# Kernel optimization log

Hardware: AMD Instinct MI355X
Metric: run time of the kernel (lower is better)

Reference implementation:

```python
import jax, jax.numpy as jnp
import numpy as np

# ---- static skeleton topology (20 edges, humanoid: spine + 2 arms + 2 legs) ----
EDGES = [(0,1),(1,2),(2,3),(3,4),(3,5),(5,6),(6,7),(7,8),(3,9),(9,10),(10,11),(11,12),
         (0,13),(13,14),(14,15),(15,16),(0,17),(17,18),(18,19),(19,20)]
SKELETON_DIST = 2
IN_PER_J, OUT_PER_J = 64, 128
KSIZE, PAD, STRIDE = 15, 7, 2
BATCH, T = 8, 4096


def _calc_edge_mat(edges):
    n = len(edges)
    INF = 100000
    m = np.full((n, n), INF, dtype=np.int64)
    np.fill_diagonal(m, 0)
    for i, a in enumerate(edges):
        for j, b in enumerate(edges):
            if a[0] in b or a[1] in b:
                m[i, j] = min(m[i, j], 1)
    for k in range(n):  # Floyd-Warshall on tiny static graph
        m = np.minimum(m, m[:, k:k+1] + m[k:k+1, :])
    return m


def _find_neighbor(edges, d):
    m = _calc_edge_mat(edges)
    n = len(edges)
    neigh = [[j for j in range(n) if m[i, j] <= d] for i in range(n)]
    global_part = list(neigh[0])
    for i in global_part:
        neigh[i].append(n)  # virtual global edge index n
    neigh.append(global_part)
    return neigh


def _build_mask(neigh, in_pj, out_pj, k):
    J = len(neigh)
    mask = np.zeros((J * out_pj, J * in_pj, k), dtype=np.float32)
    for i, nb in enumerate(neigh):
        for j in nb:
            mask[i*out_pj:(i+1)*out_pj, j*in_pj:(j+1)*in_pj, :] = 1.0
    return mask


def _build_pool_weight(edges, cpe):
    degree = [0] * 100
    for e in edges:
        degree[e[0]] += 1
        degree[e[1]] += 1
    seq_list = []
    def find_seq(j, seq):
        if degree[j] > 2 and j != 0:
            seq_list.append(seq); seq = []
        if degree[j] == 1:
            seq_list.append(seq); return
        for idx, e in enumerate(edges):
            if e[0] == j:
                find_seq(e[1], seq + [idx])
    find_seq(0, [])
    pooling = []
    for seq in seq_list:
        seq = list(seq)
        if len(seq) % 2 == 1:
            pooling.append([seq[0]]); seq = seq[1:]
        for i in range(0, len(seq), 2):
            pooling.append([seq[i], seq[i+1]])
    edge_num = len(edges) + 1
    pooling.append([edge_num - 1])
    W = np.zeros((len(pooling) * cpe, edge_num * cpe), dtype=np.float32)
    for i, pair in enumerate(pooling):
        for j in pair:
            for c in range(cpe):
                W[i*cpe + c, j*cpe + c] = 1.0 / len(pair)
    return W


def setup_inputs() -> dict:
    key = jax.random.key(0)
    k1, k2, k3 = jax.random.split(key, 3)
    J = len(EDGES) + 1  # 21 (edges + virtual global)
    in_c, out_c = J * IN_PER_J, J * OUT_PER_J  # 1344, 2688
    neigh = _find_neighbor(EDGES, SKELETON_DIST)
    mask = jnp.asarray(_build_mask(neigh, IN_PER_J, OUT_PER_J, KSIZE))
    pool_w = jnp.asarray(_build_pool_weight(EDGES, out_c // J))
    x = jax.random.normal(k1, (BATCH, in_c, T), dtype=jnp.float32)
    weight = jax.random.normal(k2, (out_c, in_c, KSIZE), dtype=jnp.float32) * 0.02
    bias = jax.random.normal(k3, (out_c,), dtype=jnp.float32) * 0.01
    return {"x": x, "weight": weight, "bias": bias, "mask": mask, "pool_w": pool_w}


def reference(x, weight, bias, mask, pool_w):
    # SkeletonConv: per-joint neighbor mask applied to dense conv1d weights
    w = weight * mask  # [out_c, in_c, K]
    xp = jnp.pad(x, ((0, 0), (0, 0), (PAD, PAD)), mode='reflect')
    y = jax.lax.conv_general_dilated(
        xp, w, window_strides=(STRIDE,), padding='VALID',
        dimension_numbers=('NCH', 'OIH', 'NCH'))
    y = y + bias[None, :, None]  # [B, out_c, T//2]
    # SkeletonPool: mean over graph-defined edge groups via matmul
    p = jnp.einsum('pc,bct->bpt', pool_w, y)
    # LeakyReLU activation as in the layer stack
    return jax.nn.leaky_relu(p, negative_slope=0.2)
```

## Files before the change

kernel.cpp:

```cpp
#include <hip/hip_runtime.h>
#include <cstdint>
#include <cstddef>

typedef unsigned short u16;
typedef unsigned int   u32;

typedef __bf16 bf16x8 __attribute__((ext_vector_type(8)));
typedef float  f32x4  __attribute__((ext_vector_type(4)));

#define AS1C(p) ((const __attribute__((address_space(1))) void*)(p))
#define AS3(p)  ((__attribute__((address_space(3))) void*)(p))

__constant__ int d_slot_jb[85] = {
  0,1,2,12,13,16,17,20,
  0,1,2,3,4,5,8,9,12,16,20,
  1,2,3,4,5,8,9,
  1,2,3,4,5,6,7,8,9,
  4,5,6,7,
  1,2,3,4,5,8,9,10,11,
  8,9,10,11,
  0,1,12,13,14,15,16,17,20,
  12,13,14,15,
  0,1,12,13,16,17,18,19,20,
  16,17,18,19,
  0,1,2,12,13,16,17
};
__constant__ int   d_gs0[12]    = {0,8,19,26,35,39,48,52,61,65,74,78};
__constant__ int   d_gnb[12]    = {8,11,7,9,4,9,4,9,4,9,4,7};
__constant__ int   d_gj0[12]    = {0,1,3,4,6,8,10,12,14,16,18,20};
__constant__ int   d_gj1[12]    = {-1,2,-1,5,7,9,11,13,15,17,19,-1};
__constant__ float d_gscale[12] = {1.f,0.5f,1.f,0.5f,0.5f,0.5f,0.5f,0.5f,0.5f,0.5f,0.5f,1.f};
__constant__ int   d_sched[12]  = {1,3,5,7,9,0,2,11,4,6,8,10};

static __device__ __forceinline__ u16 f2bf(float f) {
  union { float f; u32 u; } v; v.f = f;
  u32 r = v.u + 0x7fffu + ((v.u >> 16) & 1u);
  return (u16)(r >> 16);
}

__global__ void prep_x(const float* __restrict__ x, u16* __restrict__ xp) {
  int gid = blockIdx.x * 256 + threadIdx.x;
  if (gid >= 8 * 1344 * 514) return;
  int pc  = gid % 514;
  int row = gid / 514;
  int p   = pc * 8;
  const float* xr = x + (size_t)row * 4096;
  u16 v[8];
#pragma unroll
  for (int e = 0; e < 8; ++e) {
    int j = p + e - 7;
    j = j < 0 ? -j : (j > 4095 ? 8190 - j : j);
    v[e] = f2bf(xr[j]);
  }
  *(uint4*)(xp + (size_t)row * 4112 + p) = *(const uint4*)v;
}

__global__ void prep_w(const float* __restrict__ wt, const float* __restrict__ msk,
                       u16* __restrict__ apk) {
  int gid = blockIdx.x * 256 + threadIdx.x;
  if (gid >= 85 * 8192) return;
  int u   = gid >> 13;
  int rem = gid & 8191;
  int m   = rem >> 6;
  int c   = rem & 63;
  int g = 11;
#pragma unroll
  for (int gg = 0; gg < 11; ++gg)
    if (u >= d_gs0[gg] && u < d_gs0[gg + 1]) g = gg;
  int jb = d_slot_jb[u];
  int j0 = d_gj0[g], j1 = d_gj1[g];
  float sc = d_gscale[g];
  float m0 = msk[((size_t)(j0 * 128) * 1344 + jb * 64) * 15];
  float m1 = (j1 >= 0) ? msk[((size_t)(j1 * 128) * 1344 + jb * 64) * 15] : 0.f;
  const float* w0 = wt + ((size_t)(j0 * 128 + m) * 1344 + jb * 64 + c) * 15;
  const float* w1 = (j1 >= 0) ? wt + ((size_t)(j1 * 128 + m) * 1344 + jb * 64 + c) * 15 : w0;
  u16 v[16];
#pragma unroll
  for (int k = 0; k < 15; ++k) {
    float a = m0 * w0[k] + m1 * w1[k];
    v[k] = f2bf(a * sc);
  }
  v[15] = 0;
  uint4* dst = (uint4*)(apk + (size_t)u * 131072 + m * 1024 + c * 16);
  dst[0] = ((const uint4*)v)[0];
  dst[1] = ((const uint4*)v)[1];
}

__global__ void prep_b(const float* __restrict__ bias, float* __restrict__ bg) {
  int pc = blockIdx.x * 256 + threadIdx.x;
  if (pc >= 1536) return;
  int g = pc >> 7, m = pc & 127;
  float v = bias[d_gj0[g] * 128 + m];
  if (d_gj1[g] >= 0) v += bias[d_gj1[g] * 128 + m];
  bg[pc] = v * d_gscale[g];
}

__global__ __launch_bounds__(256, 3)
void conv_main(const u16* __restrict__ xpbf, const u16* __restrict__ apk,
               const float* __restrict__ biasg, float* __restrict__ out) {
  __shared__ __align__(16) u16 xs[64 * 280];
  __shared__ __align__(16) u16 as[128 * 64];

  const int tid = threadIdx.x;
  const int l   = tid & 63, w = tid >> 6;
  const int q   = l >> 4, lm = l & 15;
  const int wm  = w & 1, wn = w >> 1;

  const int gidx = blockIdx.x >> 7;
  const int g    = d_sched[gidx];
  const int r    = blockIdx.x & 127;
  const int b    = r >> 4;
  const int tile = r & 15;
  const int t0   = tile << 7;
  const int p0   = t0 << 1;

  const int nb = d_gnb[g];
  const int s0 = d_gs0[g];

  f32x4 acc[4][4];
#pragma unroll
  for (int i = 0; i < 4; ++i)
#pragma unroll
    for (int j = 0; j < 4; ++j)
      acc[i][j] = (f32x4){0.f, 0.f, 0.f, 0.f};

  const int as_mb = tid >> 3;
  const int as_sp = tid & 7;

  for (int s = 0; s < nb; ++s) {
    const int u  = s0 + s;
    const int jb = d_slot_jb[u];
    __syncthreads();
    {
      const u16* srow = xpbf + (size_t)(b * 1344 + jb * 64) * 4112 + p0;
      for (int i = tid; i < 64 * 34; i += 256) {
        int c  = i / 34;
        int sg = i - c * 34;
        uint4 v = *(const uint4*)(srow + (size_t)c * 4112 + sg * 8);
        *(uint4*)((char*)xs + c * 560 + sg * 16) = v;
      }
    }
    const u16* ablk = apk + (size_t)u * 131072;
    for (int kc = 0; kc < 16; ++kc) {
      __syncthreads();
#pragma unroll
      for (int ii = 0; ii < 4; ++ii) {
        int m    = ii * 32 + as_mb;
        int sloc = as_sp ^ (m & 7);
        const u16* gp = ablk + m * 1024 + kc * 64 + sloc * 8;
        __builtin_amdgcn_global_load_lds(AS1C(gp),
                                         AS3((char*)as + ii * 4096 + w * 1024),
                                         16, 0, 0);
      }
      __syncthreads();
#pragma unroll
      for (int ks = 0; ks < 2; ++ks) {
        bf16x8 af[4];
#pragma unroll
        for (int mt = 0; mt < 4; ++mt) {
          int m  = wm * 64 + mt * 16 + lm;
          int sp = (ks * 4 + q) ^ (m & 7);
          af[mt] = *(const bf16x8*)((const char*)as + m * 128 + sp * 16);
        }
        const int crow = kc * 4 + ks * 2 + (q >> 1);
        const char* xrow = (const char*)xs + crow * 560 + 16 * (q & 1);
#pragma unroll
        for (int nt = 0; nt < 4; ++nt) {
          int n = wn * 64 + nt * 16 + lm;
          const char* bp = xrow + 4 * n;
          union { u32 u[4]; bf16x8 v; } bb;
#pragma unroll
          for (int ww = 0; ww < 4; ++ww)
            bb.u[ww] = *(const u32*)(bp + 4 * ww);
#pragma unroll
          for (int mt = 0; mt < 4; ++mt)
            acc[mt][nt] = __builtin_amdgcn_mfma_f32_16x16x32_bf16(
                af[mt], bb.v, acc[mt][nt], 0, 0, 0);
        }
      }
    }
  }

  const float* bgp = biasg + g * 128 + wm * 64;
  float* outb = out + ((size_t)b * 1536 + g * 128 + wm * 64) * 2048 + t0 + wn * 64;
#pragma unroll
  for (int mt = 0; mt < 4; ++mt) {
    const f32x4 bv = *(const f32x4*)(bgp + mt * 16 + q * 4);
#pragma unroll
    for (int reg = 0; reg < 4; ++reg) {
      const float bias = bv[reg];
      const int m = mt * 16 + q * 4 + reg;
      float* orow = outb + (size_t)m * 2048 + lm;
#pragma unroll
      for (int nt = 0; nt < 4; ++nt) {
        float v = acc[mt][nt][reg] + bias;
        orow[nt * 16] = v < 0.f ? 0.2f * v : v;
      }
    }
  }
}

extern "C" void kernel_launch(void* const* d_in, const int* in_sizes, int n_in,
                              void* d_out, int out_size, void* d_ws, size_t ws_size,
                              hipStream_t stream) {
  (void)in_sizes; (void)n_in; (void)out_size; (void)ws_size;
  const float* x   = (const float*)d_in[0];
  const float* wt  = (const float*)d_in[1];
  const float* bs  = (const float*)d_in[2];
  const float* msk = (const float*)d_in[3];

  u16*   xpbf = (u16*)d_ws;
  u16*   apk  = (u16*)((char*)d_ws + 88424448);
  float* bg   = (float*)((char*)d_ws + 110706688);
  float* out  = (float*)d_out;

  prep_x<<<dim3(21588), dim3(256), 0, stream>>>(x, xpbf);
  prep_w<<<dim3(2720),  dim3(256), 0, stream>>>(wt, msk, apk);
  prep_b<<<dim3(6),     dim3(256), 0, stream>>>(bs, bg);
  conv_main<<<dim3(1536), dim3(256), 0, stream>>>(xpbf, apk, bg, out);
}
```

Baseline: 780.3 us.

## Coalesce prep_x and prep_w loads via LDS staging

prep_x now handles one row per block. It loads the row with float4 reads, packs it to bf16 in LDS, and writes the reflect-padded output using a shift-based fast path for interior chunks. prep_w now maps one wavefront to one output row (u,m), reads the 960 contiguous weights coalesced, and transposes them through LDS into the padded 16-tap layout. Both changes replace strided or scattered global reads with coalesced ones, at the cost of extra LDS traffic and a barrier per block.

```diff
diff --git a/kernel.cpp b/kernel.cpp
--- a/kernel.cpp
+++ b/kernel.cpp
@@ -37,53 +37,95 @@
   u32 r = v.u + 0x7fffu + ((v.u >> 16) & 1u);
   return (u16)(r >> 16);
 }
-
-__global__ void prep_x(const float* __restrict__ x, u16* __restrict__ xp) {
-  int gid = blockIdx.x * 256 + threadIdx.x;
-  if (gid >= 8 * 1344 * 514) return;
-  int pc  = gid % 514;
-  int row = gid / 514;
-  int p   = pc * 8;
-  const float* xr = x + (size_t)row * 4096;
-  u16 v[8];
-#pragma unroll
-  for (int e = 0; e < 8; ++e) {
-    int j = p + e - 7;
-    j = j < 0 ? -j : (j > 4095 ? 8190 - j : j);
-    v[e] = f2bf(xr[j]);
-  }
-  *(uint4*)(xp + (size_t)row * 4112 + p) = *(const uint4*)v;
-}
-
-__global__ void prep_w(const float* __restrict__ wt, const float* __restrict__ msk,
-                       u16* __restrict__ apk) {
-  int gid = blockIdx.x * 256 + threadIdx.x;
-  if (gid >= 85 * 8192) return;
-  int u   = gid >> 13;
-  int rem = gid & 8191;
-  int m   = rem >> 6;
-  int c   = rem & 63;
+static __device__ __forceinline__ u32 pk2(float lo, float hi) {
+  return (u32)f2bf(lo) | ((u32)f2bf(hi) << 16);
+}
+
+__global__ __launch_bounds__(256) void prep_x(const float* __restrict__ x,
+                                              u16* __restrict__ xp) {
+  __shared__ __align__(16) u32 lx[2048];
+  const int row = blockIdx.x;
+  const int t   = threadIdx.x;
+
+  {
+    const float4* xr4 = (const float4*)(x + (size_t)row * 4096) + t * 4;
+    float4 f0 = xr4[0], f1 = xr4[1], f2 = xr4[2], f3 = xr4[3];
+    u32 o[8];
+    o[0] = pk2(f0.x, f0.y); o[1] = pk2(f0.z, f0.w);
+    o[2] = pk2(f1.x, f1.y); o[3] = pk2(f1.z, f1.w);
+    o[4] = pk2(f2.x, f2.y); o[5] = pk2(f2.z, f2.w);
+    o[6] = pk2(f3.x, f3.y); o[7] = pk2(f3.z, f3.w);
+    ((uint4*)lx)[t * 2 + 0] = ((const uint4*)o)[0];
+    ((uint4*)lx)[t * 2 + 1] = ((const uint4*)o)[1];
+  }
+  __syncthreads();
+
+  u16* orow = xp + (size_t)row * 4112;
+  auto store_chunk = [&](int d) {
+    if (d >= 1 && d <= 511) {
+      uint4 A = ((const uint4*)lx)[d - 1];
+      u32  C = lx[4 * d];
+      uint4 o;
+      o.x = (A.x >> 16) | (A.y << 16);
+      o.y = (A.y >> 16) | (A.z << 16);
+      o.z = (A.z >> 16) | (A.w << 16);
+      o.w = (A.w >> 16) | (C << 16);
+      *(uint4*)(orow + d * 8) = o;
+    } else {
+      u32 o[4];
+#pragma unroll
+      for (int j = 0; j < 4; ++j) {
+        int p0 = d * 8 + 2 * j;
+        int s0 = p0 - 7; s0 = s0 < 0 ? -s0 : (s0 > 4095 ? 8190 - s0 : s0);
+        int s1 = p0 - 6; s1 = s1 < 0 ? -s1 : (s1 > 4095 ? 8190 - s1 : s1);
+        u32 w0 = lx[s0 >> 1], w1 = lx[s1 >> 1];
+        u32 lo = (s0 & 1) ? (w0 >> 16) : (w0 & 0xffffu);
+        u32 hi = (s1 & 1) ? (w1 >> 16) : (w1 & 0xffffu);
+        o[j] = lo | (hi << 16);
+      }
+      *(uint4*)(orow + d * 8) = ((const uint4*)o)[0];
+    }
+  };
+  store_chunk(t);
+  store_chunk(t + 256);
+  if (t < 2) store_chunk(512 + t);
+}
+
+__global__ __launch_bounds__(256) void prep_w(const float* __restrict__ wt,
+                                              const float* __restrict__ msk,
+                                              u16* __restrict__ apk) {
+  __shared__ float wls[4][1024];
+  const int t = threadIdx.x & 63, w = threadIdx.x >> 6;
+  const int wid = blockIdx.x * 4 + w;
+  const int u = wid >> 7, m = wid & 127;
   int g = 11;
 #pragma unroll
   for (int gg = 0; gg < 11; ++gg)
     if (u >= d_gs0[gg] && u < d_gs0[gg + 1]) g = gg;
-  int jb = d_slot_jb[u];
-  int j0 = d_gj0[g], j1 = d_gj1[g];
-  float sc = d_gscale[g];
-  float m0 = msk[((size_t)(j0 * 128) * 1344 + jb * 64) * 15];
-  float m1 = (j1 >= 0) ? msk[((size_t)(j1 * 128) * 1344 + jb * 64) * 15] : 0.f;
-  const float* w0 = wt + ((size_t)(j0 * 128 + m) * 1344 + jb * 64 + c) * 15;
-  const float* w1 = (j1 >= 0) ? wt + ((size_t)(j1 * 128 + m) * 1344 + jb * 64 + c) * 15 : w0;
-  u16 v[16];
+  const int jb = d_slot_jb[u];
+  const int j0 = d_gj0[g], j1 = d_gj1[g];
+  const float sc = d_gscale[g];
+  const float m0 = msk[((size_t)(j0 * 128) * 1344 + jb * 64) * 15] * sc;
+  const float m1 = (j1 >= 0) ? msk[((size_t)(j1 * 128) * 1344 + jb * 64) * 15] * sc : 0.f;
+  const float* w0 = wt + ((size_t)(j0 * 128 + m) * 1344 + jb * 64) * 15;
+  const float* w1 = (j1 >= 0) ? wt + ((size_t)(j1 * 128 + m) * 1344 + jb * 64) * 15 : w0;
+
+  float* L = wls[w];
+  L[t * 16 + 15] = 0.f;
 #pragma unroll
   for (int k = 0; k < 15; ++k) {
-    float a = m0 * w0[k] + m1 * w1[k];
-    v[k] = f2bf(a * sc);
-  }
-  v[15] = 0;
-  uint4* dst = (uint4*)(apk + (size_t)u * 131072 + m * 1024 + c * 16);
-  dst[0] = ((const uint4*)v)[0];
-  dst[1] = ((const uint4*)v)[1];
+    int i = k * 64 + t;
+    float v = m0 * w0[i] + m1 * w1[i];
+    int c = i / 15, tap = i - c * 15;
+    L[c * 16 + tap] = v;
+  }
+  __syncthreads();
+  u16 vv[16];
+#pragma unroll
+  for (int e = 0; e < 16; ++e) vv[e] = f2bf(L[t * 16 + e]);
+  uint4* dst = (uint4*)(apk + (size_t)u * 131072 + m * 1024 + t * 16);
+  dst[0] = ((const uint4*)vv)[0];
+  dst[1] = ((const uint4*)vv)[1];
 }
 
 __global__ void prep_b(const float* __restrict__ bias, float* __restrict__ bg) {
@@ -214,7 +256,7 @@
   float* bg   = (float*)((char*)d_ws + 110706688);
   float* out  = (float*)d_out;
 
-  prep_x<<<dim3(21588), dim3(256), 0, stream>>>(x, xpbf);
+  prep_x<<<dim3(10752), dim3(256), 0, stream>>>(x, xpbf);
   prep_w<<<dim3(2720),  dim3(256), 0, stream>>>(wt, msk, apk);
   prep_b<<<dim3(6),     dim3(256), 0, stream>>>(bs, bg);
   conv_main<<<dim3(1536), dim3(256), 0, stream>>>(xpbf, apk, bg, out);
```

Measured after the change: 781.9 us. No clear change (+0.2%).
